# Kernel tuning notes

Hardware: AMD Instinct MI355X
Metric: run time of the kernel (lower is better)

Reference implementation:

```python
import jax, jax.numpy as jnp
import numpy as np

D = 100          # graph size d
DIST = 10        # band distance
PI_ARG = 10.0    # args.pi
TOL = 1e-4       # args.tol
HID = 64         # hid_dim of each TApproximator
NP_ = int(HID * 0.2)   # 12 periodic units
NS_ = HID - NP_        # 52 sigmoid units

# banded off-diagonal positions in row-major order (matches reshape_B loop)
_pairs = [(r, c) for r in range(D) for c in range(D)
          if -DIST <= c - r <= DIST and r != c]
E = len(_pairs)  # = D*D - D - (D-DIST)*(D-DIST-1) = 1890
ROWS = jnp.array([p[0] for p in _pairs], dtype=jnp.int32)
COLS = jnp.array([p[1] for p in _pairs], dtype=jnp.int32)

N = 2048  # number of time points


def setup_inputs() -> dict:
    key = jax.random.key(0)
    ks = jax.random.split(key, 11)
    def lin(k, shape, fan_in):
        return jax.random.uniform(k, shape, jnp.float32, -1.0, 1.0) / np.sqrt(fan_in)
    return {
        "T":      jax.random.normal(ks[0], (N,), jnp.float32),
        "W1":     lin(ks[1], (E, NS_), 1),        # fc1 weight (input is scalar)
        "b1":     lin(ks[2], (E, NS_), 1),
        "W1p":    lin(ks[3], (E, NP_), 1),        # fc1_ weight
        "b1p":    lin(ks[4], (E, NP_), 1),
        "W2":     lin(ks[5], (E, HID, HID), HID), # fc2 weight [E, in, out]
        "b2":     lin(ks[6], (E, HID), HID),
        "W3":     lin(ks[7], (E, HID), HID),      # fc3 weight
        "b3":     lin(ks[8], (E,), HID),
        "beta":   jnp.ones((E,), jnp.float32),    # nn.Parameter([1.0]) per edge
        "bias_p": jnp.ones((E,), jnp.float32),    # nn.Parameter([1.0]) per edge
    }


def reference(T, W1, b1, W1p, b1p, W2, b2, W3, b3, beta, bias_p):
    # All E tiny MLPs evaluated as one batched pass. T: [N]
    t = T[:, None, None]                                   # [N,1,1]
    x1 = jax.nn.sigmoid(t * W1[None] + b1[None])           # [N,E,52]
    lin2 = t * W1p[None] + b1p[None]                       # [N,E,12]
    x2 = jnp.cos(beta[None, :, None] * jnp.pi * lin2 / PI_ARG
                 + bias_p[None, :, None])                  # [N,E,12]
    h = jax.nn.sigmoid(jnp.concatenate([x1, x2], axis=-1)) # [N,E,64] (double sigmoid on x1 path, as in source)
    h = jax.nn.sigmoid(jnp.einsum('neh,ehk->nek', h, W2) + b2[None])  # [N,E,64]
    out = jnp.einsum('neh,eh->ne', h, W3) + b3[None]       # [N,E]
    out = jnp.where(jnp.abs(out) < TOL, 0.0, out)          # masked_fill sparsify
    # reshape_B: scatter banded entries into [N, D, D]
    B = jnp.zeros((T.shape[0], D, D), dtype=out.dtype).at[:, ROWS, COLS].set(out)
    return B
```

## Files before the change

### kernel.cpp

```cpp
#include <hip/hip_runtime.h>
#include <hip/hip_bf16.h>
#include <stdint.h>

#define D_DIM  100
#define DISTW  10
#define E_NUM  1890
#define HID    64
#define NSIG   52
#define NPF    12
#define N_ROWS 2048
#define NHALF  1024
#define ITERS  (NHALF / 64)
#define TOLV   1e-4f
#define MAT    (D_DIM * D_DIM)
#define HALF_ELEMS (NHALF * MAT)
#define ZB     256

#define TS        1024
#define F_SCALE   (TS / 13.0f)
#define F_OFF     (TS * 0.5f + 0.5f)
#define E_SCALE   (TS / 16.0f)
#define E_CONST   (TS * 0.5f + 0.5f + 2.0f * TS)

typedef __attribute__((ext_vector_type(8))) short bf16x8;
typedef __attribute__((ext_vector_type(4))) float f32x4;

__device__ __forceinline__ float fast_exp2(float x) { return __builtin_amdgcn_exp2f(x); }
__device__ __forceinline__ float fast_rcp(float x)  { return __builtin_amdgcn_rcpf(x); }
__device__ __forceinline__ float fast_cosr(float x) { return __builtin_amdgcn_cosf(x); }

__device__ __forceinline__ float sigmoid_exact(float x) {
    return fast_rcp(1.0f + fast_exp2(x * -1.44269504f));
}

__device__ __forceinline__ short f2bf(float x) {
    __hip_bfloat16 h = __float2bfloat16(x);
    return __builtin_bit_cast(short, h);
}

__device__ __forceinline__ float dpp_sum16(float v) {
    int x;
    x = __builtin_amdgcn_update_dpp(0, __builtin_bit_cast(int, v), 0x118, 0xF, 0xF, true);
    v += __builtin_bit_cast(float, x);
    x = __builtin_amdgcn_update_dpp(0, __builtin_bit_cast(int, v), 0x114, 0xF, 0xF, true);
    v += __builtin_bit_cast(float, x);
    x = __builtin_amdgcn_update_dpp(0, __builtin_bit_cast(int, v), 0x112, 0xF, 0xF, true);
    v += __builtin_bit_cast(float, x);
    x = __builtin_amdgcn_update_dpp(0, __builtin_bit_cast(int, v), 0x111, 0xF, 0xF, true);
    v += __builtin_bit_cast(float, x);
    return v;
}

__global__ __launch_bounds__(256)
void golem_kernel(const float* __restrict__ T,   const float* __restrict__ W1,
                  const float* __restrict__ b1,  const float* __restrict__ W1p,
                  const float* __restrict__ b1p, const float* __restrict__ W2,
                  const float* __restrict__ b2,  const float* __restrict__ W3,
                  const float* __restrict__ b3,  const float* __restrict__ beta,
                  const float* __restrict__ bias_p, float* __restrict__ Bout)
{
    const int tid  = threadIdx.x;
    const int half = blockIdx.y;

    if (blockIdx.x >= E_NUM) {
        const int zb  = (int)blockIdx.x - E_NUM;
        const int per = HALF_ELEMS / ZB;
        const size_t base = (size_t)half * HALF_ELEMS + (size_t)zb * per;
        for (int off = tid * 4; off < per; off += 256 * 4) {
            const size_t i = base + off;
            const int cell = (int)(i % MAT);
            const int r = cell / D_DIM;
            const int c = cell - r * D_DIM;
            const bool fast = (c <= D_DIM - 4) && ((c + 3 < r - DISTW) || (c > r + DISTW));
            if (fast) {
                *reinterpret_cast<f32x4*>(Bout + i) = (f32x4){0.0f, 0.0f, 0.0f, 0.0f};
            } else {
                #pragma unroll
                for (int k = 0; k < 4; ++k) {
                    const size_t j = i + k;
                    const int cell2 = (int)(j % MAT);
                    const int r2 = cell2 / D_DIM;
                    const int c2 = cell2 - r2 * D_DIM;
                    const int d = c2 - r2;
                    const bool band = (d >= -DISTW) && (d <= DISTW) && (d != 0);
                    if (!band) Bout[j] = 0.0f;
                }
            }
        }
        return;
    }

    const int e    = blockIdx.x;
    const int lane = tid & 63;
    const int wave = tid >> 6;
    const int g    = lane >> 4;
    const int lm   = lane & 15;

    __shared__ float sLut[3 * TS];
    __shared__ float sTT[NHALF];
    __shared__ float sWA[HID], sWB[HID], sW3[HID], sB2[HID];
    __shared__ float sScal[1];
    __shared__ int   sRC;

    for (int i = tid; i < NHALF; i += 256) sTT[i] = T[half * NHALF + i];

    {
        const float cc1 = beta[e] * 0.05f;
        const float cc2 = bias_p[e] * 0.15915494309f;
        for (int i = tid; i < TS; i += 256) {
            float x  = (i - (TS / 2)) * (13.0f / TS);
            sLut[i]          = sigmoid_exact(sigmoid_exact(x));
            sLut[TS + i]     = sigmoid_exact(fast_cosr(fmaf(x, cc1, cc2)));
            float xe = (i - (TS / 2)) * (16.0f / TS);
            sLut[2 * TS + i] = sigmoid_exact(xe);
        }
    }

    if (tid < HID) {
        float wa, wb;
        if (tid < NSIG) { wa = W1 [e * NSIG + tid];         wb = b1 [e * NSIG + tid]; }
        else            { wa = W1p[e * NPF + (tid - NSIG)]; wb = b1p[e * NPF + (tid - NSIG)]; }
        sWA[tid] = wa; sWB[tid] = wb;
        sW3[tid] = W3[e * HID + tid];
        sB2[tid] = b2[e * HID + tid];
    }
    if (tid == 0) {
        sScal[0] = b3[e];
        int r = 0, off = 0;
        for (;;) {
            int lo = r - DISTW; if (lo < 0) lo = 0;
            int hi = r + DISTW; if (hi > D_DIM - 1) hi = D_DIM - 1;
            int cnt = hi - lo;
            if (e < off + cnt) {
                int idx = e - off;
                int c = lo + idx;
                if (c >= r) c += 1;
                sRC = r * D_DIM + c;
                break;
            }
            off += cnt; ++r;
        }
    }
    __syncthreads();

    const float* W2e = W2 + (size_t)e * (HID * HID);
    bf16x8 bfrag[2][4];
    #pragma unroll
    for (int kk = 0; kk < 2; ++kk)
        #pragma unroll
        for (int ct = 0; ct < 4; ++ct)
            #pragma unroll
            for (int j = 0; j < 8; ++j)
                bfrag[kk][ct][j] = f2bf(W2e[(8 * g + j + 32 * kk) * HID + 16 * ct + lm]);

    float colW[16], colB[16];
    #pragma unroll
    for (int kk = 0; kk < 2; ++kk)
        #pragma unroll
        for (int j = 0; j < 8; ++j) {
            int c = 8 * g + j + 32 * kk;
            colW[8 * kk + j] = sWA[c] * F_SCALE;
            colB[8 * kk + j] = fmaf(sWB[c], F_SCALE, F_OFF + ((c < NSIG) ? 0.0f : (float)TS));
        }

    float b2v[4], w3v[4];
    #pragma unroll
    for (int ct = 0; ct < 4; ++ct) {
        b2v[ct] = sB2[16 * ct + lm];
        w3v[ct] = sW3[16 * ct + lm];
    }
    const float bias3 = sScal[0];
    const int   rcoff = sRC;
    const char* lutB  = (const char*)sLut;

    for (int it = 0; it < ITERS; ++it) {
        const int n0 = half * NHALF + it * 64 + wave * 16;
        const float t = sTT[it * 64 + wave * 16 + lm];

        bf16x8 afrag[2];
        #pragma unroll
        for (int q = 0; q < 2; ++q)
            #pragma unroll
            for (int j = 0; j < 8; ++j) {
                float x = fmaf(t, colW[8 * q + j], colB[8 * q + j]);
                uint32_t bi = ((uint32_t)x) << 2;
                afrag[q][j] = f2bf(*(const float*)(lutB + bi));
            }

        f32x4 acc[4];
        #pragma unroll
        for (int ct = 0; ct < 4; ++ct)
            acc[ct] = (f32x4){b2v[ct], b2v[ct], b2v[ct], b2v[ct]};
        #pragma unroll
        for (int ct = 0; ct < 4; ++ct) {
            acc[ct] = __builtin_amdgcn_mfma_f32_16x16x32_bf16(afrag[0], bfrag[0][ct], acc[ct], 0, 0, 0);
            acc[ct] = __builtin_amdgcn_mfma_f32_16x16x32_bf16(afrag[1], bfrag[1][ct], acc[ct], 0, 0, 0);
        }

        float p[4];
        #pragma unroll
        for (int reg = 0; reg < 4; ++reg) {
            float s = 0.0f;
            #pragma unroll
            for (int ct = 0; ct < 4; ++ct) {
                float x = fmaf(acc[ct][reg], E_SCALE, E_CONST);
                uint32_t bi = ((uint32_t)x) << 2;
                s = fmaf(*(const float*)(lutB + bi), w3v[ct], s);
            }
            p[reg] = dpp_sum16(s);
        }

        if (lm == 15) {
            #pragma unroll
            for (int r = 0; r < 4; ++r) {
                float out = p[r] + bias3;
                if (fabsf(out) < TOLV) out = 0.0f;
                int row = n0 + 4 * g + r;
                Bout[(size_t)row * MAT + rcoff] = out;
            }
        }
    }
}

extern "C" void kernel_launch(void* const* d_in, const int* in_sizes, int n_in,
                              void* d_out, int out_size, void* d_ws, size_t ws_size,
                              hipStream_t stream) {
    const float* T      = (const float*)d_in[0];
    const float* W1     = (const float*)d_in[1];
    const float* b1     = (const float*)d_in[2];
    const float* W1p    = (const float*)d_in[3];
    const float* b1p    = (const float*)d_in[4];
    const float* W2     = (const float*)d_in[5];
    const float* b2     = (const float*)d_in[6];
    const float* W3     = (const float*)d_in[7];
    const float* b3     = (const float*)d_in[8];
    const float* beta   = (const float*)d_in[9];
    const float* bias_p = (const float*)d_in[10];
    float* Bout = (float*)d_out;

    golem_kernel<<<dim3(E_NUM + ZB, 2), dim3(256), 0, stream>>>(
        T, W1, b1, W1p, b1p, W2, b2, W3, b3, beta, bias_p, Bout);
}
```

Before: 125.7 us.

## Process all time rows per edge block with software-pipelined feature/MFMA stages

Drops the two-way split over time halves, so each edge block builds its LUT and loads its W2 fragments once and covers all 2048 time rows. The loop is software-pipelined with two A-fragment buffers: features for the next tile are computed while the current tile's MFMAs and epilogue run. Feature and epilogue index arithmetic is packed into two-wide and four-wide float vector ops. The grid halves to about 2400 blocks, which removes duplicated per-block setup but gives less parallelism per block and uses more registers.

```diff
diff --git a/kernel.cpp b/kernel.cpp
--- a/kernel.cpp
+++ b/kernel.cpp
@@ -9,12 +9,12 @@
 #define NSIG   52
 #define NPF    12
 #define N_ROWS 2048
-#define NHALF  1024
-#define ITERS  (NHALF / 64)
+#define ITERS  (N_ROWS / 64)
 #define TOLV   1e-4f
 #define MAT    (D_DIM * D_DIM)
-#define HALF_ELEMS (NHALF * MAT)
-#define ZB     256
+#define TOT_ELEMS (N_ROWS * MAT)
+#define ZB     512
+#define ZPER   (TOT_ELEMS / ZB)
 
 #define TS        1024
 #define F_SCALE   (TS / 13.0f)
@@ -24,6 +24,7 @@
 
 typedef __attribute__((ext_vector_type(8))) short bf16x8;
 typedef __attribute__((ext_vector_type(4))) float f32x4;
+typedef __attribute__((ext_vector_type(2))) float f32x2;
 
 __device__ __forceinline__ float fast_exp2(float x) { return __builtin_amdgcn_exp2f(x); }
 __device__ __forceinline__ float fast_rcp(float x)  { return __builtin_amdgcn_rcpf(x); }
@@ -50,6 +51,53 @@
     v += __builtin_bit_cast(float, x);
     return v;
 }
+
+#define FEAT_PAIR(AF, K, TV) {                                              \
+    f32x2 x2 = (f32x2){(TV), (TV)} * cw[K] + cb[K];                         \
+    uint32_t b0 = ((uint32_t)x2.x) << 2;                                    \
+    uint32_t b1 = ((uint32_t)x2.y) << 2;                                    \
+    AF[(K) >> 2][2 * ((K) & 3)]     = f2bf(*(const float*)(lutB + b0));     \
+    AF[(K) >> 2][2 * ((K) & 3) + 1] = f2bf(*(const float*)(lutB + b1)); }
+#define FEAT16(AF, TV) { FEAT_PAIR(AF,0,TV) FEAT_PAIR(AF,1,TV)              \
+    FEAT_PAIR(AF,2,TV) FEAT_PAIR(AF,3,TV) FEAT_PAIR(AF,4,TV)                \
+    FEAT_PAIR(AF,5,TV) FEAT_PAIR(AF,6,TV) FEAT_PAIR(AF,7,TV) }
+
+#define MM8(ACC, AF) {                                                      \
+    _Pragma("unroll")                                                       \
+    for (int ct = 0; ct < 4; ++ct)                                          \
+        ACC[ct] = (f32x4){b2v[ct], b2v[ct], b2v[ct], b2v[ct]};              \
+    _Pragma("unroll")                                                       \
+    for (int ct = 0; ct < 4; ++ct) {                                        \
+        ACC[ct] = __builtin_amdgcn_mfma_f32_16x16x32_bf16(AF[0], bfrag[0][ct], ACC[ct], 0, 0, 0); \
+        ACC[ct] = __builtin_amdgcn_mfma_f32_16x16x32_bf16(AF[1], bfrag[1][ct], ACC[ct], 0, 0, 0); \
+    } }
+
+#define EPI(ACC, N0) {                                                      \
+    f32x4 ix[4];                                                            \
+    _Pragma("unroll")                                                       \
+    for (int ct = 0; ct < 4; ++ct)                                          \
+        ix[ct] = ACC[ct] * (f32x4){E_SCALE,E_SCALE,E_SCALE,E_SCALE}         \
+               + (f32x4){E_CONST,E_CONST,E_CONST,E_CONST};                  \
+    float p[4];                                                             \
+    _Pragma("unroll")                                                       \
+    for (int reg = 0; reg < 4; ++reg) {                                     \
+        float s = 0.0f;                                                     \
+        _Pragma("unroll")                                                   \
+        for (int ct = 0; ct < 4; ++ct) {                                    \
+            uint32_t bi = ((uint32_t)ix[ct][reg]) << 2;                     \
+            s = fmaf(*(const float*)(lutB + bi), w3v[ct], s);               \
+        }                                                                   \
+        p[reg] = dpp_sum16(s);                                              \
+    }                                                                       \
+    if (lm == 15) {                                                         \
+        _Pragma("unroll")                                                   \
+        for (int r = 0; r < 4; ++r) {                                       \
+            float out = p[r] + bias3;                                       \
+            if (fabsf(out) < TOLV) out = 0.0f;                              \
+            int row = (N0) + 4 * g + r;                                     \
+            Bout[(size_t)row * MAT + rcoff] = out;                          \
+        }                                                                   \
+    } }
 
 __global__ __launch_bounds__(256)
 void golem_kernel(const float* __restrict__ T,   const float* __restrict__ W1,
@@ -59,14 +107,12 @@
                   const float* __restrict__ b3,  const float* __restrict__ beta,
                   const float* __restrict__ bias_p, float* __restrict__ Bout)
 {
-    const int tid  = threadIdx.x;
-    const int half = blockIdx.y;
+    const int tid = threadIdx.x;
 
     if (blockIdx.x >= E_NUM) {
-        const int zb  = (int)blockIdx.x - E_NUM;
-        const int per = HALF_ELEMS / ZB;
-        const size_t base = (size_t)half * HALF_ELEMS + (size_t)zb * per;
-        for (int off = tid * 4; off < per; off += 256 * 4) {
+        const int zb = (int)blockIdx.x - E_NUM;
+        const size_t base = (size_t)zb * ZPER;
+        for (int off = tid * 4; off < ZPER; off += 256 * 4) {
             const size_t i = base + off;
             const int cell = (int)(i % MAT);
             const int r = cell / D_DIM;
@@ -97,12 +143,12 @@
     const int lm   = lane & 15;
 
     __shared__ float sLut[3 * TS];
-    __shared__ float sTT[NHALF];
+    __shared__ float sTT[N_ROWS];
     __shared__ float sWA[HID], sWB[HID], sW3[HID], sB2[HID];
     __shared__ float sScal[1];
     __shared__ int   sRC;
 
-    for (int i = tid; i < NHALF; i += 256) sTT[i] = T[half * NHALF + i];
+    for (int i = tid; i < N_ROWS; i += 256) sTT[i] = T[i];
 
     {
         const float cc1 = beta[e] * 0.05f;
@@ -153,15 +199,16 @@
             for (int j = 0; j < 8; ++j)
                 bfrag[kk][ct][j] = f2bf(W2e[(8 * g + j + 32 * kk) * HID + 16 * ct + lm]);
 
-    float colW[16], colB[16];
+    f32x2 cw[8], cb[8];
     #pragma unroll
-    for (int kk = 0; kk < 2; ++kk)
-        #pragma unroll
-        for (int j = 0; j < 8; ++j) {
-            int c = 8 * g + j + 32 * kk;
-            colW[8 * kk + j] = sWA[c] * F_SCALE;
-            colB[8 * kk + j] = fmaf(sWB[c], F_SCALE, F_OFF + ((c < NSIG) ? 0.0f : (float)TS));
-        }
+    for (int k = 0; k < 8; ++k) {
+        int q = k >> 2, j0 = 2 * (k & 3);
+        int c0 = 8 * g + j0 + 32 * q;
+        float base0 = F_OFF + ((c0     < NSIG) ? 0.0f : (float)TS);
+        float base1 = F_OFF + ((c0 + 1 < NSIG) ? 0.0f : (float)TS);
+        cw[k] = (f32x2){sWA[c0] * F_SCALE, sWA[c0 + 1] * F_SCALE};
+        cb[k] = (f32x2){fmaf(sWB[c0], F_SCALE, base0), fmaf(sWB[c0 + 1], F_SCALE, base1)};
+    }
 
     float b2v[4], w3v[4];
     #pragma unroll
@@ -172,52 +219,29 @@
     const float bias3 = sScal[0];
     const int   rcoff = sRC;
     const char* lutB  = (const char*)sLut;
-
-    for (int it = 0; it < ITERS; ++it) {
-        const int n0 = half * NHALF + it * 64 + wave * 16;
-        const float t = sTT[it * 64 + wave * 16 + lm];
-
-        bf16x8 afrag[2];
-        #pragma unroll
-        for (int q = 0; q < 2; ++q)
-            #pragma unroll
-            for (int j = 0; j < 8; ++j) {
-                float x = fmaf(t, colW[8 * q + j], colB[8 * q + j]);
-                uint32_t bi = ((uint32_t)x) << 2;
-                afrag[q][j] = f2bf(*(const float*)(lutB + bi));
+    const int   rbase = wave * 16;
+
+    bf16x8 afA[2], afB[2];
+    {
+        float t0 = sTT[rbase + lm];
+        FEAT16(afA, t0);
+    }
+    for (int it = 0; it < ITERS; it += 2) {
+        {
+            f32x4 acc[4];
+            MM8(acc, afA);
+            float tB = sTT[(it + 1) * 64 + rbase + lm];
+            FEAT16(afB, tB);
+            EPI(acc, it * 64 + rbase);
+        }
+        {
+            f32x4 acc[4];
+            MM8(acc, afB);
+            if (it < ITERS - 2) {
+                float tA = sTT[(it + 2) * 64 + rbase + lm];
+                FEAT16(afA, tA);
             }
-
-        f32x4 acc[4];
-        #pragma unroll
-        for (int ct = 0; ct < 4; ++ct)
-            acc[ct] = (f32x4){b2v[ct], b2v[ct], b2v[ct], b2v[ct]};
-        #pragma unroll
-        for (int ct = 0; ct < 4; ++ct) {
-            acc[ct] = __builtin_amdgcn_mfma_f32_16x16x32_bf16(afrag[0], bfrag[0][ct], acc[ct], 0, 0, 0);
-            acc[ct] = __builtin_amdgcn_mfma_f32_16x16x32_bf16(afrag[1], bfrag[1][ct], acc[ct], 0, 0, 0);
-        }
-
-        float p[4];
-        #pragma unroll
-        for (int reg = 0; reg < 4; ++reg) {
-            float s = 0.0f;
-            #pragma unroll
-            for (int ct = 0; ct < 4; ++ct) {
-                float x = fmaf(acc[ct][reg], E_SCALE, E_CONST);
-                uint32_t bi = ((uint32_t)x) << 2;
-                s = fmaf(*(const float*)(lutB + bi), w3v[ct], s);
-            }
-            p[reg] = dpp_sum16(s);
-        }
-
-        if (lm == 15) {
-            #pragma unroll
-            for (int r = 0; r < 4; ++r) {
-                float out = p[r] + bias3;
-                if (fabsf(out) < TOLV) out = 0.0f;
-                int row = n0 + 4 * g + r;
-                Bout[(size_t)row * MAT + rcoff] = out;
-            }
+            EPI(acc, (it + 1) * 64 + rbase);
         }
     }
 }
@@ -238,6 +262,6 @@
     const float* bias_p = (const float*)d_in[10];
     float* Bout = (float*)d_out;
 
-    golem_kernel<<<dim3(E_NUM + ZB, 2), dim3(256), 0, stream>>>(
+    golem_kernel<<<dim3(E_NUM + ZB), dim3(256), 0, stream>>>(
         T, W1, b1, W1p, b1p, W2, b2, W3, b3, beta, bias_p, Bout);
 }
```

Result: slower. 134.4 us (+6.9%).

## Fold -log2e into W2, compute output sigmoid directly, pack LUT gathers with perm

Applied to the files above, without the earlier changes.

Replaces the third sigmoid LUT with a direct exp2+rcp sigmoid, folding the -log2(e) scale into the bf16 W2 fragments and the b2 bias. The first-layer LUT stores values already rounded to bf16, so two gathered floats are packed into one register with a byte perm. Feature address math is done two columns at a time with packed float2 ops. T is now read straight from global memory rather than staged in shared memory, and launch bounds ask for 4 blocks per CU. This cuts LDS size and gather/convert work, but adds transcendental instructions in the inner loop.

```diff
diff --git a/kernel.cpp b/kernel.cpp
--- a/kernel.cpp
+++ b/kernel.cpp
@@ -19,18 +19,18 @@
 #define TS        1024
 #define F_SCALE   (TS / 13.0f)
 #define F_OFF     (TS * 0.5f + 0.5f)
-#define E_SCALE   (TS / 16.0f)
-#define E_CONST   (TS * 0.5f + 0.5f + 2.0f * TS)
+#define NEGLOG2E  (-1.44269504f)
 
 typedef __attribute__((ext_vector_type(8))) short bf16x8;
 typedef __attribute__((ext_vector_type(4))) float f32x4;
+typedef __attribute__((ext_vector_type(2))) float f32x2;
 
 __device__ __forceinline__ float fast_exp2(float x) { return __builtin_amdgcn_exp2f(x); }
 __device__ __forceinline__ float fast_rcp(float x)  { return __builtin_amdgcn_rcpf(x); }
 __device__ __forceinline__ float fast_cosr(float x) { return __builtin_amdgcn_cosf(x); }
 
 __device__ __forceinline__ float sigmoid_exact(float x) {
-    return fast_rcp(1.0f + fast_exp2(x * -1.44269504f));
+    return fast_rcp(1.0f + fast_exp2(x * NEGLOG2E));
 }
 
 __device__ __forceinline__ short f2bf(float x) {
@@ -38,6 +38,11 @@
     return __builtin_bit_cast(short, h);
 }
 
+__device__ __forceinline__ float prebf(float x) {
+    uint32_t u = ((uint32_t)(uint16_t)f2bf(x)) << 16;
+    return __builtin_bit_cast(float, u);
+}
+
 __device__ __forceinline__ float dpp_sum16(float v) {
     int x;
     x = __builtin_amdgcn_update_dpp(0, __builtin_bit_cast(int, v), 0x118, 0xF, 0xF, true);
@@ -51,7 +56,20 @@
     return v;
 }
 
-__global__ __launch_bounds__(256)
+union ABfrag { bf16x8 v; uint32_t u[4]; };
+
+#define FEAT_PAIR(AF, K, TV) {                                              \
+    f32x2 x2 = (f32x2){(TV), (TV)} * cw[K] + cb[K];                         \
+    uint32_t b0 = ((uint32_t)x2.x) << 2;                                    \
+    uint32_t b1 = ((uint32_t)x2.y) << 2;                                    \
+    uint32_t g0 = *(const uint32_t*)(lutB + b0);                            \
+    uint32_t g1 = *(const uint32_t*)(lutB + b1);                            \
+    AF[(K) >> 2].u[(K) & 3] = __builtin_amdgcn_perm(g1, g0, 0x07060302); }
+#define FEAT16(AF, TV) { FEAT_PAIR(AF,0,TV) FEAT_PAIR(AF,1,TV)              \
+    FEAT_PAIR(AF,2,TV) FEAT_PAIR(AF,3,TV) FEAT_PAIR(AF,4,TV)                \
+    FEAT_PAIR(AF,5,TV) FEAT_PAIR(AF,6,TV) FEAT_PAIR(AF,7,TV) }
+
+__global__ __launch_bounds__(256, 4)
 void golem_kernel(const float* __restrict__ T,   const float* __restrict__ W1,
                   const float* __restrict__ b1,  const float* __restrict__ W1p,
                   const float* __restrict__ b1p, const float* __restrict__ W2,
@@ -96,23 +114,18 @@
     const int g    = lane >> 4;
     const int lm   = lane & 15;
 
-    __shared__ float sLut[3 * TS];
-    __shared__ float sTT[NHALF];
+    __shared__ float sLut[2 * TS];
     __shared__ float sWA[HID], sWB[HID], sW3[HID], sB2[HID];
     __shared__ float sScal[1];
     __shared__ int   sRC;
-
-    for (int i = tid; i < NHALF; i += 256) sTT[i] = T[half * NHALF + i];
 
     {
         const float cc1 = beta[e] * 0.05f;
         const float cc2 = bias_p[e] * 0.15915494309f;
         for (int i = tid; i < TS; i += 256) {
             float x  = (i - (TS / 2)) * (13.0f / TS);
-            sLut[i]          = sigmoid_exact(sigmoid_exact(x));
-            sLut[TS + i]     = sigmoid_exact(fast_cosr(fmaf(x, cc1, cc2)));
-            float xe = (i - (TS / 2)) * (16.0f / TS);
-            sLut[2 * TS + i] = sigmoid_exact(xe);
+            sLut[i]      = prebf(sigmoid_exact(sigmoid_exact(x)));
+            sLut[TS + i] = prebf(sigmoid_exact(fast_cosr(fmaf(x, cc1, cc2))));
         }
     }
 
@@ -151,41 +164,35 @@
         for (int ct = 0; ct < 4; ++ct)
             #pragma unroll
             for (int j = 0; j < 8; ++j)
-                bfrag[kk][ct][j] = f2bf(W2e[(8 * g + j + 32 * kk) * HID + 16 * ct + lm]);
-
-    float colW[16], colB[16];
+                bfrag[kk][ct][j] = f2bf(W2e[(8 * g + j + 32 * kk) * HID + 16 * ct + lm] * NEGLOG2E);
+
+    f32x2 cw[8], cb[8];
     #pragma unroll
-    for (int kk = 0; kk < 2; ++kk)
-        #pragma unroll
-        for (int j = 0; j < 8; ++j) {
-            int c = 8 * g + j + 32 * kk;
-            colW[8 * kk + j] = sWA[c] * F_SCALE;
-            colB[8 * kk + j] = fmaf(sWB[c], F_SCALE, F_OFF + ((c < NSIG) ? 0.0f : (float)TS));
-        }
+    for (int k = 0; k < 8; ++k) {
+        int q = k >> 2, j0 = 2 * (k & 3);
+        int c0 = 8 * g + j0 + 32 * q;
+        float base0 = F_OFF + ((c0     < NSIG) ? 0.0f : (float)TS);
+        float base1 = F_OFF + ((c0 + 1 < NSIG) ? 0.0f : (float)TS);
+        cw[k] = (f32x2){sWA[c0] * F_SCALE, sWA[c0 + 1] * F_SCALE};
+        cb[k] = (f32x2){fmaf(sWB[c0], F_SCALE, base0), fmaf(sWB[c0 + 1], F_SCALE, base1)};
+    }
 
     float b2v[4], w3v[4];
     #pragma unroll
     for (int ct = 0; ct < 4; ++ct) {
-        b2v[ct] = sB2[16 * ct + lm];
+        b2v[ct] = sB2[16 * ct + lm] * NEGLOG2E;
         w3v[ct] = sW3[16 * ct + lm];
     }
     const float bias3 = sScal[0];
     const int   rcoff = sRC;
     const char* lutB  = (const char*)sLut;
+    const float* Tg = T + half * NHALF + wave * 16 + lm;
 
     for (int it = 0; it < ITERS; ++it) {
-        const int n0 = half * NHALF + it * 64 + wave * 16;
-        const float t = sTT[it * 64 + wave * 16 + lm];
-
-        bf16x8 afrag[2];
-        #pragma unroll
-        for (int q = 0; q < 2; ++q)
-            #pragma unroll
-            for (int j = 0; j < 8; ++j) {
-                float x = fmaf(t, colW[8 * q + j], colB[8 * q + j]);
-                uint32_t bi = ((uint32_t)x) << 2;
-                afrag[q][j] = f2bf(*(const float*)(lutB + bi));
-            }
+        const float t = Tg[it * 64];
+
+        ABfrag af[2];
+        FEAT16(af, t);
 
         f32x4 acc[4];
         #pragma unroll
@@ -193,8 +200,8 @@
             acc[ct] = (f32x4){b2v[ct], b2v[ct], b2v[ct], b2v[ct]};
         #pragma unroll
         for (int ct = 0; ct < 4; ++ct) {
-            acc[ct] = __builtin_amdgcn_mfma_f32_16x16x32_bf16(afrag[0], bfrag[0][ct], acc[ct], 0, 0, 0);
-            acc[ct] = __builtin_amdgcn_mfma_f32_16x16x32_bf16(afrag[1], bfrag[1][ct], acc[ct], 0, 0, 0);
+            acc[ct] = __builtin_amdgcn_mfma_f32_16x16x32_bf16(af[0].v, bfrag[0][ct], acc[ct], 0, 0, 0);
+            acc[ct] = __builtin_amdgcn_mfma_f32_16x16x32_bf16(af[1].v, bfrag[1][ct], acc[ct], 0, 0, 0);
         }
 
         float p[4];
@@ -202,11 +209,8 @@
         for (int reg = 0; reg < 4; ++reg) {
             float s = 0.0f;
             #pragma unroll
-            for (int ct = 0; ct < 4; ++ct) {
-                float x = fmaf(acc[ct][reg], E_SCALE, E_CONST);
-                uint32_t bi = ((uint32_t)x) << 2;
-                s = fmaf(*(const float*)(lutB + bi), w3v[ct], s);
-            }
+            for (int ct = 0; ct < 4; ++ct)
+                s = fmaf(fast_rcp(1.0f + fast_exp2(acc[ct][reg])), w3v[ct], s);
             p[reg] = dpp_sum16(s);
         }
 
@@ -215,7 +219,7 @@
             for (int r = 0; r < 4; ++r) {
                 float out = p[r] + bias3;
                 if (fabsf(out) < TOLV) out = 0.0f;
-                int row = n0 + 4 * g + r;
+                int row = half * NHALF + it * 64 + wave * 16 + 4 * g + r;
                 Bout[(size_t)row * MAT + rcoff] = out;
             }
         }
```

Result: faster. 123.1 us (-2.1%).
